# Performance work log

Measured on AMD Instinct MI355X. Metric: run time of the kernel, lower is better.

The kernel has to match this reference:

```python
import jax, jax.numpy as jnp
import numpy as np

B, C, V = 1024, 512, 256  # batch, num_conjunctions, num_variables


def setup_inputs() -> dict:
    key = jax.random.key(0)
    k1, k2, k3 = jax.random.split(key, 3)
    x0 = jax.random.uniform(k1, (B, V), dtype=jnp.float32)
    # torch init: conj = 1 - 2*rand  -> uniform in (-1, 1)
    conjunctions = 1.0 - 2.0 * jax.random.uniform(k2, (C, 2 * V), dtype=jnp.float32)
    # rw = 10 - 20*rand -> uniform in (-10, 10)
    rule_weights = 10.0 - 20.0 * jax.random.uniform(k3, (C,), dtype=jnp.float32)
    return {"x0": x0, "conjunctions": conjunctions, "rule_weights": rule_weights}


def reference(x0, conjunctions, rule_weights):
    mu = jax.nn.sigmoid(conjunctions)            # (C, 2V)
    x = jnp.concatenate((x0, 1.0 - x0), axis=1)  # (B, 2V)
    # fuzzy-AND: broadcast mul-add then min over literal axis
    x_pot = mu[None, :, :] * x[:, None, :] + (1.0 - mu)[None, :, :]  # (B, C, 2V)
    fit = jnp.min(x_pot, axis=-1)                # (B, C)
    return 5.0 + jnp.sum(rule_weights * fit, axis=-1)  # (B,)
```

## Files before the change

kernel.cpp:

```cpp
#include <hip/hip_runtime.h>


#define B_    1024
#define C_    512
#define V_    256
#define TWOV  512

#define BPB    8
#define NBG    (B_ / BPB)
#define NCH    4

typedef float f32x4 __attribute__((ext_vector_type(4)));

__global__ __launch_bounds__(256) void k_prep(const float* __restrict__ conj,
                                              float2* __restrict__ muT2,
                                              float* __restrict__ out) {
    const int c = blockIdx.x;
    const int v = threadIdx.x;
    if (c < 4) out[c * 256 + v] = 5.0f;
    float z1 = conj[(size_t)c * TWOV + v];
    float z2 = conj[(size_t)c * TWOV + V_ + v];
    float m1 = 1.0f / (1.0f + __expf(-z1));
    float m2 = 1.0f / (1.0f + __expf(-z2));
    muT2[(size_t)(v >> 1) * (2 * C_) + c * 2 + (v & 1)] = make_float2(m1, m2);
}

__global__ __launch_bounds__(512, 4) void k_main(const float* __restrict__ x0,
                                                 const f32x4* __restrict__ muT4,
                                                 const float* __restrict__ rw,
                                                 float* __restrict__ out) {
    const int tid  = threadIdx.x;
    const int lane = tid & 63;
    const int wave = tid >> 6;
    const int bg   = blockIdx.x;
    const int chunk= blockIdx.y;
    const int cA   = chunk * 128 + lane;
    const int vq   = wave * 8;

    __shared__ f32x4 xs4[BPB * V_ / 4];
    __shared__ float red[8 * 64 * 17];

    {
        const f32x4* xg = reinterpret_cast<const f32x4*>(x0 + (size_t)bg * BPB * V_);
        xs4[tid] = xg[tid];
    }

    const f32x4* pA  = muT4 + (size_t)(wave * 16) * C_ + cA;
    const f32x4* pA1 = pA + C_;

    float mA[BPB], mB[BPB];
#pragma unroll
    for (int i = 0; i < BPB; ++i) { mA[i] = 0.0f; mB[i] = 0.0f; }

    f32x4 A0a, A1a, B0a, B1a, A0b, A1b, B0b, B1b, A0c, A1c, B0c, B1c;

#define ISSUE(A0, A1, Bq0, Bq1) do { \
    asm volatile("global_load_dwordx4 %0, %1, off"             : "=v"(A0)  : "v"(pA));  \
    asm volatile("global_load_dwordx4 %0, %1, off offset:1024" : "=v"(Bq0) : "v"(pA));  \
    asm volatile("global_load_dwordx4 %0, %1, off"             : "=v"(A1)  : "v"(pA1)); \
    asm volatile("global_load_dwordx4 %0, %1, off offset:1024" : "=v"(Bq1) : "v"(pA1)); \
    pA += 2 * C_; pA1 += 2 * C_; } while (0)

    ISSUE(A0a, A1a, B0a, B1a);
    ISSUE(A0b, A1b, B0b, B1b);

    __syncthreads();

#define COMPUTE(q, A0, A1, Bq0, Bq1) do { \
    _Pragma("unroll") \
    for (int bi = 0; bi < BPB; ++bi) { \
        f32x4 xc = xs4[bi * 64 + vq + (q)]; \
        float ma = mA[bi], mb = mB[bi]; \
        ma = fmaxf(fmaxf(__builtin_fmaf(-A0.x,  xc.x, A0.x),  A0.y  * xc.x), ma); \
        ma = fmaxf(fmaxf(__builtin_fmaf(-A0.z,  xc.y, A0.z),  A0.w  * xc.y), ma); \
        ma = fmaxf(fmaxf(__builtin_fmaf(-A1.x,  xc.z, A1.x),  A1.y  * xc.z), ma); \
        ma = fmaxf(fmaxf(__builtin_fmaf(-A1.z,  xc.w, A1.z),  A1.w  * xc.w), ma); \
        mb = fmaxf(fmaxf(__builtin_fmaf(-Bq0.x, xc.x, Bq0.x), Bq0.y * xc.x), mb); \
        mb = fmaxf(fmaxf(__builtin_fmaf(-Bq0.z, xc.y, Bq0.z), Bq0.w * xc.y), mb); \
        mb = fmaxf(fmaxf(__builtin_fmaf(-Bq1.x, xc.z, Bq1.x), Bq1.y * xc.z), mb); \
        mb = fmaxf(fmaxf(__builtin_fmaf(-Bq1.z, xc.w, Bq1.z), Bq1.w * xc.w), mb); \
        mA[bi] = ma; mB[bi] = mb; \
    } } while (0)

#define QSTEP(q, CA0, CA1, CB0, CB1, NA0, NA1, NB0, NB1) do { \
    ISSUE(NA0, NA1, NB0, NB1); \
    asm volatile("s_waitcnt vmcnt(8)" : "+v"(CA0), "+v"(CA1), "+v"(CB0), "+v"(CB1)); \
    COMPUTE(q, CA0, CA1, CB0, CB1); } while (0)

    QSTEP(0, A0a, A1a, B0a, B1a,  A0c, A1c, B0c, B1c);
    QSTEP(1, A0b, A1b, B0b, B1b,  A0a, A1a, B0a, B1a);
    QSTEP(2, A0c, A1c, B0c, B1c,  A0b, A1b, B0b, B1b);
    QSTEP(3, A0a, A1a, B0a, B1a,  A0c, A1c, B0c, B1c);
    QSTEP(4, A0b, A1b, B0b, B1b,  A0a, A1a, B0a, B1a);
    QSTEP(5, A0c, A1c, B0c, B1c,  A0b, A1b, B0b, B1b);
    asm volatile("s_waitcnt vmcnt(4)" : "+v"(A0a), "+v"(A1a), "+v"(B0a), "+v"(B1a));
    COMPUTE(6, A0a, A1a, B0a, B1a);
    asm volatile("s_waitcnt vmcnt(0)" : "+v"(A0b), "+v"(A1b), "+v"(B0b), "+v"(B1b));
    COMPUTE(7, A0b, A1b, B0b, B1b);

#undef QSTEP
#undef COMPUTE
#undef ISSUE

#pragma unroll
    for (int bi = 0; bi < BPB; ++bi) {
        red[(wave * 64 + lane) * 17 + bi * 2 + 0] = mA[bi];
        red[(wave * 64 + lane) * 17 + bi * 2 + 1] = mB[bi];
    }
    __syncthreads();

    if (wave < 2) {
        const float rwc = rw[chunk * 128 + wave * 64 + lane];
        float con0, con1, con2, con3, con4, con5, con6, con7;
#define FIN(bi, CON) do { \
        float mm = red[(0 * 64 + lane) * 17 + (bi) * 2 + wave]; \
        _Pragma("unroll") \
        for (int wv = 1; wv < 8; ++wv) \
            mm = fmaxf(mm, red[(wv * 64 + lane) * 17 + (bi) * 2 + wave]); \
        float v = rwc * (1.0f - mm); \
        v += __shfl_xor(v, 1, 64);  v += __shfl_xor(v, 2, 64); \
        v += __shfl_xor(v, 4, 64);  v += __shfl_xor(v, 8, 64); \
        v += __shfl_xor(v, 16, 64); v += __shfl_xor(v, 32, 64); \
        CON = v; } while (0)
        FIN(0, con0); FIN(1, con1); FIN(2, con2); FIN(3, con3);
        FIN(4, con4); FIN(5, con5); FIN(6, con6); FIN(7, con7);
#undef FIN
        float t0 = (lane & 1) ? con1 : con0;
        float t1 = (lane & 1) ? con3 : con2;
        float t2 = (lane & 1) ? con5 : con4;
        float t3 = (lane & 1) ? con7 : con6;
        float u0 = (lane & 2) ? t1 : t0;
        float u1 = (lane & 2) ? t3 : t2;
        float sel = (lane & 4) ? u1 : u0;
        if (lane < 8)
            atomicAdd(&out[bg * BPB + lane], sel);
    }
}

__global__ __launch_bounds__(256) void k_naive(const float* __restrict__ x0,
                                               const float* __restrict__ conj,
                                               const float* __restrict__ rw,
                                               float* __restrict__ out) {
    int b = blockIdx.x;
    int t = threadIdx.x;
    __shared__ float red[256];
    float acc = 0.0f;
    for (int c = t; c < C_; c += 256) {
        float mm = 0.0f;
        for (int v = 0; v < V_; ++v) {
            float mu1 = 1.0f / (1.0f + expf(-conj[(size_t)c * TWOV + v]));
            float mu2 = 1.0f / (1.0f + expf(-conj[(size_t)c * TWOV + V_ + v]));
            float x = x0[(size_t)b * V_ + v];
            mm = fmaxf(mm, fmaxf(mu1 * (1.0f - x), mu2 * x));
        }
        acc += rw[c] * (1.0f - mm);
    }
    red[t] = acc;
    __syncthreads();
    for (int s = 128; s > 0; s >>= 1) {
        if (t < s) red[t] += red[t + s];
        __syncthreads();
    }
    if (t == 0) out[b] = 5.0f + red[0];
}

extern "C" void kernel_launch(void* const* d_in, const int* in_sizes, int n_in,
                              void* d_out, int out_size, void* d_ws, size_t ws_size,
                              hipStream_t stream) {
    const float* x0   = (const float*)d_in[0];
    const float* conj = (const float*)d_in[1];
    const float* rw   = (const float*)d_in[2];
    float* out = (float*)d_out;

    const size_t mu_floats = (size_t)(V_ / 2) * C_ * 4;
    const size_t need = mu_floats * sizeof(float);

    if (ws_size < need) {
        k_naive<<<B_, 256, 0, stream>>>(x0, conj, rw, out);
        return;
    }

    f32x4* muT4 = (f32x4*)d_ws;

    k_prep<<<C_, 256, 0, stream>>>(conj, (float2*)muT4, out);
    dim3 grid(NBG, NCH);
    k_main<<<grid, 512, 0, stream>>>(x0, muT4, rw, out);
}
```

Baseline: 22.86 us.

## Switch fuzzy-AND inner loop to packed fp16 multiply/max

Mu values and x/(1-x) are converted to packed half-precision pairs, and the inner min/max loop uses v_pk_mul_f16 and v_pk_max_f16, so each instruction handles two literals. This also halves the size of the mu workspace and the memory traffic for it. The hand-written triple-buffered asm loads are replaced by a simpler one-step prefetch, and the prep kernel layout is changed to match. The cost is fp16 rounding in the fit values, which can hurt accuracy once they are multiplied by rule weights as large as 10 and summed over 512 rules.

After: 20.96 us. 8.3% less time.

```diff
diff --git a/kernel.cpp b/kernel.cpp
--- a/kernel.cpp
+++ b/kernel.cpp
@@ -10,23 +10,38 @@
 #define NBG    (B_ / BPB)
 #define NCH    4
 
-typedef float f32x4 __attribute__((ext_vector_type(4)));
-
-__global__ __launch_bounds__(256) void k_prep(const float* __restrict__ conj,
-                                              float2* __restrict__ muT2,
+typedef float    f32x4 __attribute__((ext_vector_type(4)));
+typedef _Float16 h16x2 __attribute__((ext_vector_type(2)));
+
+__device__ __forceinline__ float sigf(float z) {
+    return 1.0f / (1.0f + __expf(-z));
+}
+__device__ __forceinline__ float packh2(float a, float b) {
+    h16x2 h; h.x = (_Float16)a; h.y = (_Float16)b;
+    return __builtin_bit_cast(float, h);
+}
+
+#define PKMUL(D, A, Bq) asm("v_pk_mul_f16 %0, %1, %2" : "=v"(D) : "v"(A), "v"(Bq))
+#define PKMAX(ACC, T)   asm("v_pk_max_f16 %0, %0, %1" : "+v"(ACC) : "v"(T))
+
+__global__ __launch_bounds__(512) void k_prep(const float* __restrict__ conj,
+                                              float4* __restrict__ muH,
                                               float* __restrict__ out) {
-    const int c = blockIdx.x;
-    const int v = threadIdx.x;
-    if (c < 4) out[c * 256 + v] = 5.0f;
-    float z1 = conj[(size_t)c * TWOV + v];
-    float z2 = conj[(size_t)c * TWOV + V_ + v];
-    float m1 = 1.0f / (1.0f + __expf(-z1));
-    float m2 = 1.0f / (1.0f + __expf(-z2));
-    muT2[(size_t)(v >> 1) * (2 * C_) + c * 2 + (v & 1)] = make_float2(m1, m2);
+    const int vq = blockIdx.x;
+    const int c  = threadIdx.x;
+    if (vq < 2) out[vq * 512 + c] = 5.0f;
+    const float* row = conj + (size_t)c * TWOV;
+    const int v = vq * 4;
+    float4 r;
+    r.x = packh2(sigf(row[v + 0]),      sigf(row[v + 1]));
+    r.y = packh2(sigf(row[v + 2]),      sigf(row[v + 3]));
+    r.z = packh2(sigf(row[V_ + v + 0]), sigf(row[V_ + v + 1]));
+    r.w = packh2(sigf(row[V_ + v + 2]), sigf(row[V_ + v + 3]));
+    muH[(size_t)vq * C_ + c] = r;
 }
 
 __global__ __launch_bounds__(512, 4) void k_main(const float* __restrict__ x0,
-                                                 const f32x4* __restrict__ muT4,
+                                                 const float4* __restrict__ muH,
                                                  const float* __restrict__ rw,
                                                  float* __restrict__ out) {
     const int tid  = threadIdx.x;
@@ -35,72 +50,87 @@
     const int bg   = blockIdx.x;
     const int chunk= blockIdx.y;
     const int cA   = chunk * 128 + lane;
-    const int vq   = wave * 8;
-
-    __shared__ f32x4 xs4[BPB * V_ / 4];
-    __shared__ float red[8 * 64 * 17];
+    const int vq0  = wave * 8;
+
+    __shared__ float4 xs4[BPB * 64];
+    __shared__ float  red[8 * 64 * 17];
 
     {
-        const f32x4* xg = reinterpret_cast<const f32x4*>(x0 + (size_t)bg * BPB * V_);
-        xs4[tid] = xg[tid];
-    }
-
-    const f32x4* pA  = muT4 + (size_t)(wave * 16) * C_ + cA;
-    const f32x4* pA1 = pA + C_;
+        const int b = tid >> 6, vq = tid & 63;
+        float4 xv = *reinterpret_cast<const float4*>(
+            x0 + (size_t)(bg * BPB + b) * V_ + vq * 4);
+        float4 pk;
+        pk.x = packh2(xv.x, xv.y);
+        pk.y = packh2(xv.z, xv.w);
+        pk.z = packh2(1.0f - xv.x, 1.0f - xv.y);
+        pk.w = packh2(1.0f - xv.z, 1.0f - xv.w);
+        xs4[tid] = pk;
+    }
+
+    const float4* p = muH + (size_t)vq0 * C_ + cA;
+
+    float accA[BPB], accB[BPB];
+#pragma unroll
+    for (int i = 0; i < BPB; ++i) { accA[i] = 0.0f; accB[i] = 0.0f; }
+
+    float4 MA = p[0];
+    float4 MB = p[64];
+
+    __syncthreads();
+
+#define PAIR(XC, bi, MAr, MBr) do { \
+    float t0, t1, t2, t3; \
+    PKMUL(t0, MAr.x, XC.z);    \
+    PKMUL(t1, MAr.z, XC.x);    \
+    PKMUL(t2, MAr.y, XC.w);    \
+    PKMUL(t3, MAr.w, XC.y);    \
+    PKMAX(accA[bi], t0); PKMAX(accA[bi], t1); \
+    PKMAX(accA[bi], t2); PKMAX(accA[bi], t3); \
+    PKMUL(t0, MBr.x, XC.z);    \
+    PKMUL(t1, MBr.z, XC.x); \
+    PKMUL(t2, MBr.y, XC.w); \
+    PKMUL(t3, MBr.w, XC.y); \
+    PKMAX(accB[bi], t0); PKMAX(accB[bi], t1); \
+    PKMAX(accB[bi], t2); PKMAX(accB[bi], t3); \
+    } while (0)
+
+#pragma unroll
+    for (int q = 0; q < 8; ++q) {
+        float4 xc0 = xs4[0 * 64 + vq0 + q];
+        float4 xc1 = xs4[1 * 64 + vq0 + q];
+        float4 xc2 = xs4[2 * 64 + vq0 + q];
+        float4 xc3 = xs4[3 * 64 + vq0 + q];
+        float4 xc4 = xs4[4 * 64 + vq0 + q];
+        float4 xc5 = xs4[5 * 64 + vq0 + q];
+        float4 xc6 = xs4[6 * 64 + vq0 + q];
+        float4 xc7 = xs4[7 * 64 + vq0 + q];
+        float4 NA, NB;
+        if (q < 7) {
+            NA = p[(size_t)(q + 1) * C_];
+            NB = p[(size_t)(q + 1) * C_ + 64];
+        }
+        asm volatile("" : "+v"(MA.x), "+v"(MA.y), "+v"(MA.z), "+v"(MA.w),
+                          "+v"(MB.x), "+v"(MB.y), "+v"(MB.z), "+v"(MB.w));
+        PAIR(xc0, 0, MA, MB);
+        PAIR(xc1, 1, MA, MB);
+        PAIR(xc2, 2, MA, MB);
+        PAIR(xc3, 3, MA, MB);
+        PAIR(xc4, 4, MA, MB);
+        PAIR(xc5, 5, MA, MB);
+        PAIR(xc6, 6, MA, MB);
+        PAIR(xc7, 7, MA, MB);
+        if (q < 7) { MA = NA; MB = NB; }
+    }
+#undef PAIR
 
     float mA[BPB], mB[BPB];
 #pragma unroll
-    for (int i = 0; i < BPB; ++i) { mA[i] = 0.0f; mB[i] = 0.0f; }
-
-    f32x4 A0a, A1a, B0a, B1a, A0b, A1b, B0b, B1b, A0c, A1c, B0c, B1c;
-
-#define ISSUE(A0, A1, Bq0, Bq1) do { \
-    asm volatile("global_load_dwordx4 %0, %1, off"             : "=v"(A0)  : "v"(pA));  \
-    asm volatile("global_load_dwordx4 %0, %1, off offset:1024" : "=v"(Bq0) : "v"(pA));  \
-    asm volatile("global_load_dwordx4 %0, %1, off"             : "=v"(A1)  : "v"(pA1)); \
-    asm volatile("global_load_dwordx4 %0, %1, off offset:1024" : "=v"(Bq1) : "v"(pA1)); \
-    pA += 2 * C_; pA1 += 2 * C_; } while (0)
-
-    ISSUE(A0a, A1a, B0a, B1a);
-    ISSUE(A0b, A1b, B0b, B1b);
-
-    __syncthreads();
-
-#define COMPUTE(q, A0, A1, Bq0, Bq1) do { \
-    _Pragma("unroll") \
-    for (int bi = 0; bi < BPB; ++bi) { \
-        f32x4 xc = xs4[bi * 64 + vq + (q)]; \
-        float ma = mA[bi], mb = mB[bi]; \
-        ma = fmaxf(fmaxf(__builtin_fmaf(-A0.x,  xc.x, A0.x),  A0.y  * xc.x), ma); \
-        ma = fmaxf(fmaxf(__builtin_fmaf(-A0.z,  xc.y, A0.z),  A0.w  * xc.y), ma); \
-        ma = fmaxf(fmaxf(__builtin_fmaf(-A1.x,  xc.z, A1.x),  A1.y  * xc.z), ma); \
-        ma = fmaxf(fmaxf(__builtin_fmaf(-A1.z,  xc.w, A1.z),  A1.w  * xc.w), ma); \
-        mb = fmaxf(fmaxf(__builtin_fmaf(-Bq0.x, xc.x, Bq0.x), Bq0.y * xc.x), mb); \
-        mb = fmaxf(fmaxf(__builtin_fmaf(-Bq0.z, xc.y, Bq0.z), Bq0.w * xc.y), mb); \
-        mb = fmaxf(fmaxf(__builtin_fmaf(-Bq1.x, xc.z, Bq1.x), Bq1.y * xc.z), mb); \
-        mb = fmaxf(fmaxf(__builtin_fmaf(-Bq1.z, xc.w, Bq1.z), Bq1.w * xc.w), mb); \
-        mA[bi] = ma; mB[bi] = mb; \
-    } } while (0)
-
-#define QSTEP(q, CA0, CA1, CB0, CB1, NA0, NA1, NB0, NB1) do { \
-    ISSUE(NA0, NA1, NB0, NB1); \
-    asm volatile("s_waitcnt vmcnt(8)" : "+v"(CA0), "+v"(CA1), "+v"(CB0), "+v"(CB1)); \
-    COMPUTE(q, CA0, CA1, CB0, CB1); } while (0)
-
-    QSTEP(0, A0a, A1a, B0a, B1a,  A0c, A1c, B0c, B1c);
-    QSTEP(1, A0b, A1b, B0b, B1b,  A0a, A1a, B0a, B1a);
-    QSTEP(2, A0c, A1c, B0c, B1c,  A0b, A1b, B0b, B1b);
-    QSTEP(3, A0a, A1a, B0a, B1a,  A0c, A1c, B0c, B1c);
-    QSTEP(4, A0b, A1b, B0b, B1b,  A0a, A1a, B0a, B1a);
-    QSTEP(5, A0c, A1c, B0c, B1c,  A0b, A1b, B0b, B1b);
-    asm volatile("s_waitcnt vmcnt(4)" : "+v"(A0a), "+v"(A1a), "+v"(B0a), "+v"(B1a));
-    COMPUTE(6, A0a, A1a, B0a, B1a);
-    asm volatile("s_waitcnt vmcnt(0)" : "+v"(A0b), "+v"(A1b), "+v"(B0b), "+v"(B1b));
-    COMPUTE(7, A0b, A1b, B0b, B1b);
-
-#undef QSTEP
-#undef COMPUTE
-#undef ISSUE
+    for (int bi = 0; bi < BPB; ++bi) {
+        h16x2 ha = __builtin_bit_cast(h16x2, accA[bi]);
+        h16x2 hb = __builtin_bit_cast(h16x2, accB[bi]);
+        mA[bi] = fmaxf((float)ha.x, (float)ha.y);
+        mB[bi] = fmaxf((float)hb.x, (float)hb.y);
+    }
 
 #pragma unroll
     for (int bi = 0; bi < BPB; ++bi) {
@@ -172,17 +202,16 @@
     const float* rw   = (const float*)d_in[2];
     float* out = (float*)d_out;
 
-    const size_t mu_floats = (size_t)(V_ / 2) * C_ * 4;
-    const size_t need = mu_floats * sizeof(float);
+    const size_t need = (size_t)64 * C_ * 16;
 
     if (ws_size < need) {
         k_naive<<<B_, 256, 0, stream>>>(x0, conj, rw, out);
         return;
     }
 
-    f32x4* muT4 = (f32x4*)d_ws;
-
-    k_prep<<<C_, 256, 0, stream>>>(conj, (float2*)muT4, out);
+    float4* muH = (float4*)d_ws;
+
+    k_prep<<<64, 512, 0, stream>>>(conj, muH, out);
     dim3 grid(NBG, NCH);
-    k_main<<<grid, 512, 0, stream>>>(x0, muT4, rw, out);
-}
+    k_main<<<grid, 512, 0, stream>>>(x0, muH, rw, out);
+}
```
